# Kernel tuning notes

Hardware: AMD Instinct MI355X
Metric: run time of the kernel (lower is better)

## Reference

```python
import jax, jax.numpy as jnp
import numpy as np

B, S, DIN, DOUT, R, NL, T = 4, 4096, 1024, 1024, 16, 8, 4

def setup_inputs() -> dict:
    key = jax.random.key(0)
    k1, k2, k3, k4, k5 = jax.random.split(key, 5)
    return {
        "x": jax.random.normal(k1, (B, S, DIN), dtype=jnp.float32),
        "W": jax.random.normal(k2, (DOUT, DIN), dtype=jnp.float32) * 0.02,
        "bias": jax.random.normal(k3, (DOUT,), dtype=jnp.float32) * 0.02,
        "lora_A": jax.random.normal(k4, (NL, R, DIN), dtype=jnp.float32) * 0.02,
        "lora_B": jax.random.normal(k5, (NL, DOUT, R), dtype=jnp.float32) * 0.02,
        "tuner_index": jnp.arange(T, dtype=jnp.int64) if jax.config.jax_enable_x64 else jnp.arange(T, dtype=jnp.int32),
    }

def reference(x, W, bias, lora_A, lora_B, tuner_index):
    # Per adapter ti: F.linear(x, W + B_ti @ A_ti, bias)
    # == x @ W.T + (x @ A_ti.T) @ B_ti.T + bias  (fused low-rank form, same math)
    A = lora_A[tuner_index]   # [T, r, Din]
    Bm = lora_B[tuner_index]  # [T, Dout, r]
    base = jnp.einsum('bsd,od->bso', x, W) + bias          # [B, S, Dout]
    low = jnp.einsum('bsd,trd->tbsr', x, A)                # [T, B, S, r]
    delta = jnp.einsum('tbsr,tor->tbso', low, Bm)          # [T, B, S, Dout]
    return base[None, ...] + delta                         # [T, B, S, Dout]
```

## Files before the change

kernel.cpp:

```cpp
#include <hip/hip_runtime.h>


typedef __attribute__((ext_vector_type(8))) _Float16 f16x8;
typedef __attribute__((ext_vector_type(4))) float f32x4;
typedef __attribute__((ext_vector_type(4))) unsigned short us4;
typedef __attribute__((ext_vector_type(8))) unsigned short us8;

namespace {
constexpr int kM = 16384, kDin = 1024, kDout = 1024, kR = 16, kT = 4;
constexpr size_t OFF_XF  = 0;
constexpr size_t OFF_WF  = 33554432;
constexpr size_t OFF_LOW = 35651584;
}

__device__ inline unsigned short f2h(float f) {
  _Float16 h = (_Float16)f;
  return __builtin_bit_cast(unsigned short, h);
}
__device__ inline void gload_lds16(const void* g, void* l) {
  __builtin_amdgcn_global_load_lds(
      (const __attribute__((address_space(1))) unsigned int*)g,
      (__attribute__((address_space(3))) unsigned int*)l, 16, 0, 0);
}
__device__ inline f32x4 mfma_f16(f16x8 a, f16x8 b, f32x4 c) {
  return __builtin_amdgcn_mfma_f32_16x16x32_f16(a, b, c, 0, 0, 0);
}

__global__ __launch_bounds__(256) void lora_low(const float* __restrict__ x,
                                                const float* __restrict__ W,
                                                const float* __restrict__ A,
                                                const int* __restrict__ tuner,
                                                unsigned short* __restrict__ lowb,
                                                unsigned short* __restrict__ xf,
                                                unsigned short* __restrict__ wf) {
  {
    const int idx = blockIdx.x * 256 + threadIdx.x;
#pragma unroll
    for (int p = 0; p < 2; ++p) {
      const int j = idx + p * 131072;
      const float4 v = ((const float4*)W)[j];
      us4 h;
      h[0] = f2h(v.x); h[1] = f2h(v.y); h[2] = f2h(v.z); h[3] = f2h(v.w);
      ((us4*)wf)[j] = h;
    }
  }

  __shared__ float xs[64][34];
  __shared__ float as[64][66];
  const int tid = threadIdx.x;
  const int i0  = blockIdx.x * 32;
  const int tx  = tid & 15;
  const int ty  = tid >> 4;
  float acc[2][4] = {{0.f, 0.f, 0.f, 0.f}, {0.f, 0.f, 0.f, 0.f}};

  for (int kt = 0; kt < kDin; kt += 64) {
    __syncthreads();
#pragma unroll
    for (int p = 0; p < 2; ++p) {
      const int f = tid + p * 256;
      const int row = f >> 4, kq = (f & 15) * 4;
      const float4 v = *(const float4*)(x + (size_t)(i0 + row) * kDin + kt + kq);
      xs[kq + 0][row] = v.x; xs[kq + 1][row] = v.y;
      xs[kq + 2][row] = v.z; xs[kq + 3][row] = v.w;
      us4 h;
      h[0] = f2h(v.x); h[1] = f2h(v.y); h[2] = f2h(v.z); h[3] = f2h(v.w);
      *(us4*)(xf + (size_t)(i0 + row) * kDin + kt + kq) = h;
    }
#pragma unroll
    for (int p = 0; p < 4; ++p) {
      const int f = tid + p * 256;
      const int ar = f >> 4, kq = (f & 15) * 4;
      const int ti = tuner[ar >> 4];
      const float4 v = *(const float4*)(A + ((size_t)ti * kR + (ar & 15)) * kDin + kt + kq);
      as[kq + 0][ar] = v.x; as[kq + 1][ar] = v.y;
      as[kq + 2][ar] = v.z; as[kq + 3][ar] = v.w;
    }
    __syncthreads();
#pragma unroll 8
    for (int k = 0; k < 64; ++k) {
      const float a0 = xs[k][ty * 2], a1 = xs[k][ty * 2 + 1];
      const float b0 = as[k][tx * 4], b1 = as[k][tx * 4 + 1];
      const float b2 = as[k][tx * 4 + 2], b3 = as[k][tx * 4 + 3];
      acc[0][0] += a0 * b0; acc[0][1] += a0 * b1; acc[0][2] += a0 * b2; acc[0][3] += a0 * b3;
      acc[1][0] += a1 * b0; acc[1][1] += a1 * b1; acc[1][2] += a1 * b2; acc[1][3] += a1 * b3;
    }
  }
#pragma unroll
  for (int ii = 0; ii < 2; ++ii) {
    us4 o;
#pragma unroll
    for (int j = 0; j < 4; ++j) o[j] = f2h(acc[ii][j]);
    *(us4*)(lowb + ((size_t)(tx >> 2) * kM + i0 + ty * 2 + ii) * kR + (tx & 3) * 4) = o;
  }
}

__global__ __launch_bounds__(512) void lora_main(
    const unsigned short* __restrict__ xf, const unsigned short* __restrict__ wf,
    const float* __restrict__ bias, const float* __restrict__ Bm,
    const int* __restrict__ tuner, const unsigned short* __restrict__ lowb,
    float* __restrict__ out) {
  __shared__ __align__(16) unsigned char smem[49152];
  const int tid  = threadIdx.x;
  const int lane = tid & 63;
  const int w    = tid >> 6;

  const int swz = ((int)blockIdx.x & 7) * 64 + ((int)blockIdx.x >> 3);
  const int bm = swz >> 2, bn = swz & 3;
  const size_t i0 = (size_t)bm * 128, j0 = (size_t)bn * 256;
  const int wm = w >> 2, wn = w & 3;

  const int chsw = ((lane & 3) ^ ((lane >> 3) & 3)) * 8;
  const unsigned short* gsrc_q[3];
  int ldsoff_q[3];
#pragma unroll
  for (int q = 0; q < 3; ++q) {
    const int c = 3 * w + q;
    const bool isA = c < 8;
    const size_t rowb = (isA ? i0 + c * 16 : j0 + (c - 8) * 16) + (lane >> 2);
    gsrc_q[q] = (isA ? xf : wf) + rowb * kDin + chsw;
    ldsoff_q[q] = c * 1024;
  }

  f32x4 acc[4][4];
#pragma unroll
  for (int n = 0; n < 4; ++n)
#pragma unroll
    for (int m = 0; m < 4; ++m) acc[n][m] = (f32x4){0.f, 0.f, 0.f, 0.f};

  const int kg = lane >> 4;
  const int rl = lane & 15;
  const int csw = kg ^ ((rl >> 1) & 3);
  const int rdA = (wm * 64 + rl) * 64 + csw * 16;
  const int rdB = 8192 + (wn * 64 + rl) * 64 + csw * 16;

  auto compute_step = [&](const unsigned char* B0) {
    f16x8 a[4], b[4];
#pragma unroll
    for (int m = 0; m < 4; ++m) a[m] = *(const f16x8*)(B0 + rdA + m * 1024);
#pragma unroll
    for (int n = 0; n < 4; ++n) b[n] = *(const f16x8*)(B0 + rdB + n * 1024);
    __builtin_amdgcn_s_setprio(1);
#pragma unroll
    for (int n = 0; n < 4; ++n)
#pragma unroll
      for (int m = 0; m < 4; ++m)
        acc[n][m] = mfma_f16(b[n], a[m], acc[n][m]);
    __builtin_amdgcn_s_setprio(0);
  };

#pragma unroll
  for (int q = 0; q < 3; ++q)
    gload_lds16(gsrc_q[q], smem + ldsoff_q[q]);

  for (int s = 0; s < 31; ++s) {
    const int p = s & 1;
    {
      unsigned char* dst = smem + (p ^ 1) * 24576;
      const int ko = (s + 1) * 32;
#pragma unroll
      for (int q = 0; q < 3; ++q)
        gload_lds16(gsrc_q[q] + ko, dst + ldsoff_q[q]);
    }
    asm volatile("s_waitcnt vmcnt(3)" ::: "memory");
    __builtin_amdgcn_s_barrier();
    asm volatile("" ::: "memory");
    compute_step(smem + p * 24576);
    asm volatile("s_waitcnt lgkmcnt(0)" ::: "memory");
    __builtin_amdgcn_s_barrier();
    asm volatile("" ::: "memory");
  }
  asm volatile("s_waitcnt vmcnt(0)" ::: "memory");
  __builtin_amdgcn_s_barrier();
  asm volatile("" ::: "memory");
  compute_step(smem + 24576);

#pragma unroll
  for (int n = 0; n < 4; ++n) {
    const f32x4 bv = *(const f32x4*)(bias + j0 + wn * 64 + n * 16 + kg * 4);
#pragma unroll
    for (int m = 0; m < 4; ++m)
#pragma unroll
      for (int r = 0; r < 4; ++r) acc[n][m][r] += bv[r];
  }

  {
    const us8 z = {0, 0, 0, 0, 0, 0, 0, 0};
    if (tid < 128) {
      *(us8*)(smem + 4096 + tid * 32) = z;
      *(us8*)(smem + 4096 + tid * 32 + 16) = z;
    } else if (tid < 384) {
      *(us8*)(smem + 16384 + (tid - 128) * 32) = z;
      *(us8*)(smem + 16384 + (tid - 128) * 32 + 16) = z;
    }
  }

  for (int t = 0; t < kT; ++t) {
    __syncthreads();
    {
      const int row = tid >> 1, half = tid & 1;
      if (tid < 256) {
        const us8 lv = *(const us8*)(lowb + ((size_t)t * kM + i0 + row) * kR + half * 8);
        *(us8*)(smem + half * 2048 + row * 16) = lv;
      }
      const int ti = tuner[t];
      const float* bp = Bm + ((size_t)ti * kDout + j0 + row) * kR + half * 8;
      const float4 m0 = *(const float4*)bp;
      const float4 m1 = *(const float4*)(bp + 4);
      us8 mv;
      mv[0] = f2h(m0.x); mv[1] = f2h(m0.y); mv[2] = f2h(m0.z); mv[3] = f2h(m0.w);
      mv[4] = f2h(m1.x); mv[5] = f2h(m1.y); mv[6] = f2h(m1.z); mv[7] = f2h(m1.w);
      *(us8*)(smem + 8192 + half * 4096 + row * 16) = mv;
    }
    __syncthreads();

    f16x8 lf[4], mf[4];
#pragma unroll
    for (int m = 0; m < 4; ++m)
      lf[m] = *(const f16x8*)(smem + kg * 2048 + (wm * 64 + m * 16 + rl) * 16);
#pragma unroll
    for (int n = 0; n < 4; ++n)
      mf[n] = *(const f16x8*)(smem + 8192 + kg * 4096 + (wn * 64 + n * 16 + rl) * 16);

#pragma unroll
    for (int n = 0; n < 4; ++n)
#pragma unroll
      for (int m = 0; m < 4; ++m) {
        const f32x4 d = mfma_f16(mf[n], lf[m], acc[n][m]);
        const size_t row = (size_t)t * kM + i0 + wm * 64 + m * 16 + rl;
        const int    col = (int)j0 + wn * 64 + n * 16 + kg * 4;
        __builtin_nontemporal_store(d, (f32x4*)(out + row * kDout + col));
      }
  }
}

extern "C" void kernel_launch(void* const* d_in, const int* in_sizes, int n_in,
                              void* d_out, int out_size, void* d_ws, size_t ws_size,
                              hipStream_t stream) {
  const float* x    = (const float*)d_in[0];
  const float* W    = (const float*)d_in[1];
  const float* bias = (const float*)d_in[2];
  const float* lA   = (const float*)d_in[3];
  const float* lB   = (const float*)d_in[4];
  const int*   ti   = (const int*)d_in[5];
  float* out = (float*)d_out;

  unsigned char* ws = (unsigned char*)d_ws;
  unsigned short* xfp  = (unsigned short*)(ws + OFF_XF);
  unsigned short* wfp  = (unsigned short*)(ws + OFF_WF);
  unsigned short* lowb = (unsigned short*)(ws + OFF_LOW);

  lora_low<<<kM / 32, 256, 0, stream>>>(x, W, lA, ti, lowb, xfp, wfp);
  lora_main<<<512, 512, 0, stream>>>(xfp, wfp, bias, lB, ti, lowb, out);
}
```

Before: 161.5 us.

## Split main GEMM into 128x128 tiles with 256-thread blocks and two tiles each

The main kernel drops from 512-thread blocks computing a 128x256 output tile to 256-thread blocks that loop over two 128x128 tiles in sequence. Shared memory shrinks from 48KB to 32KB and the launch bounds ask for two blocks per CU, aiming for better occupancy and overlap between blocks. The low-rank kernel also switches to vectorized float2/float4 LDS reads with a padded A tile. In exchange, the x tile is loaded twice per block (once per column tile) and each wave keeps a 64x64 accumulator tile, so register pressure stays high.

```diff
diff --git a/kernel.cpp b/kernel.cpp
--- a/kernel.cpp
+++ b/kernel.cpp
@@ -46,7 +46,7 @@
   }
 
   __shared__ float xs[64][34];
-  __shared__ float as[64][66];
+  __shared__ float as[64][68];
   const int tid = threadIdx.x;
   const int i0  = blockIdx.x * 32;
   const int tx  = tid & 15;
@@ -76,13 +76,14 @@
       as[kq + 2][ar] = v.z; as[kq + 3][ar] = v.w;
     }
     __syncthreads();
-#pragma unroll 8
+#pragma unroll 4
     for (int k = 0; k < 64; ++k) {
-      const float a0 = xs[k][ty * 2], a1 = xs[k][ty * 2 + 1];
-      const float b0 = as[k][tx * 4], b1 = as[k][tx * 4 + 1];
-      const float b2 = as[k][tx * 4 + 2], b3 = as[k][tx * 4 + 3];
-      acc[0][0] += a0 * b0; acc[0][1] += a0 * b1; acc[0][2] += a0 * b2; acc[0][3] += a0 * b3;
-      acc[1][0] += a1 * b0; acc[1][1] += a1 * b1; acc[1][2] += a1 * b2; acc[1][3] += a1 * b3;
+      const float2 xv = *(const float2*)&xs[k][ty * 2];
+      const float4 av = *(const float4*)&as[k][tx * 4];
+      acc[0][0] += xv.x * av.x; acc[0][1] += xv.x * av.y;
+      acc[0][2] += xv.x * av.z; acc[0][3] += xv.x * av.w;
+      acc[1][0] += xv.y * av.x; acc[1][1] += xv.y * av.y;
+      acc[1][2] += xv.y * av.z; acc[1][3] += xv.y * av.w;
     }
   }
 #pragma unroll
@@ -94,142 +95,143 @@
   }
 }
 
-__global__ __launch_bounds__(512) void lora_main(
+__global__ __launch_bounds__(256, 2) void lora_main(
     const unsigned short* __restrict__ xf, const unsigned short* __restrict__ wf,
     const float* __restrict__ bias, const float* __restrict__ Bm,
     const int* __restrict__ tuner, const unsigned short* __restrict__ lowb,
     float* __restrict__ out) {
-  __shared__ __align__(16) unsigned char smem[49152];
+  __shared__ __align__(16) unsigned char smem[32768];
   const int tid  = threadIdx.x;
   const int lane = tid & 63;
   const int w    = tid >> 6;
 
   const int swz = ((int)blockIdx.x & 7) * 64 + ((int)blockIdx.x >> 3);
-  const int bm = swz >> 2, bn = swz & 3;
-  const size_t i0 = (size_t)bm * 128, j0 = (size_t)bn * 256;
-  const int wm = w >> 2, wn = w & 3;
+  const int bm = swz >> 2, bn2 = swz & 3;
+  const size_t i0 = (size_t)bm * 128;
+  const int wm = w >> 1, wn = w & 1;
 
   const int chsw = ((lane & 3) ^ ((lane >> 3) & 3)) * 8;
-  const unsigned short* gsrc_q[3];
-  int ldsoff_q[3];
-#pragma unroll
-  for (int q = 0; q < 3; ++q) {
-    const int c = 3 * w + q;
-    const bool isA = c < 8;
-    const size_t rowb = (isA ? i0 + c * 16 : j0 + (c - 8) * 16) + (lane >> 2);
-    gsrc_q[q] = (isA ? xf : wf) + rowb * kDin + chsw;
-    ldsoff_q[q] = c * 1024;
-  }
-
-  f32x4 acc[4][4];
-#pragma unroll
-  for (int n = 0; n < 4; ++n)
-#pragma unroll
-    for (int m = 0; m < 4; ++m) acc[n][m] = (f32x4){0.f, 0.f, 0.f, 0.f};
-
   const int kg = lane >> 4;
   const int rl = lane & 15;
   const int csw = kg ^ ((rl >> 1) & 3);
   const int rdA = (wm * 64 + rl) * 64 + csw * 16;
   const int rdB = 8192 + (wn * 64 + rl) * 64 + csw * 16;
 
-  auto compute_step = [&](const unsigned char* B0) {
-    f16x8 a[4], b[4];
-#pragma unroll
-    for (int m = 0; m < 4; ++m) a[m] = *(const f16x8*)(B0 + rdA + m * 1024);
-#pragma unroll
-    for (int n = 0; n < 4; ++n) b[n] = *(const f16x8*)(B0 + rdB + n * 1024);
-    __builtin_amdgcn_s_setprio(1);
+#pragma unroll 1
+  for (int tt = 0; tt < 2; ++tt) {
+    const size_t j0 = (size_t)(bn2 + 4 * tt) * 128;
+
+    const unsigned short* gsrc_q[4];
+    int ldsoff_q[4];
+#pragma unroll
+    for (int q = 0; q < 4; ++q) {
+      const int c = 4 * w + q;
+      const bool isA = c < 8;
+      const size_t rowb = (isA ? i0 + c * 16 : j0 + (c - 8) * 16) + (lane >> 2);
+      gsrc_q[q] = (isA ? xf : wf) + rowb * kDin + chsw;
+      ldsoff_q[q] = c * 1024;
+    }
+
+    f32x4 acc[4][4];
 #pragma unroll
     for (int n = 0; n < 4; ++n)
 #pragma unroll
-      for (int m = 0; m < 4; ++m)
-        acc[n][m] = mfma_f16(b[n], a[m], acc[n][m]);
-    __builtin_amdgcn_s_setprio(0);
-  };
-
-#pragma unroll
-  for (int q = 0; q < 3; ++q)
-    gload_lds16(gsrc_q[q], smem + ldsoff_q[q]);
-
-  for (int s = 0; s < 31; ++s) {
-    const int p = s & 1;
-    {
-      unsigned char* dst = smem + (p ^ 1) * 24576;
-      const int ko = (s + 1) * 32;
-#pragma unroll
-      for (int q = 0; q < 3; ++q)
-        gload_lds16(gsrc_q[q] + ko, dst + ldsoff_q[q]);
-    }
-    asm volatile("s_waitcnt vmcnt(3)" ::: "memory");
+      for (int m = 0; m < 4; ++m) acc[n][m] = (f32x4){0.f, 0.f, 0.f, 0.f};
+
+    auto compute_step = [&](const unsigned char* B0) {
+      f16x8 a[4], b[4];
+#pragma unroll
+      for (int m = 0; m < 4; ++m) a[m] = *(const f16x8*)(B0 + rdA + m * 1024);
+#pragma unroll
+      for (int n = 0; n < 4; ++n) b[n] = *(const f16x8*)(B0 + rdB + n * 1024);
+      __builtin_amdgcn_s_setprio(1);
+#pragma unroll
+      for (int n = 0; n < 4; ++n)
+#pragma unroll
+        for (int m = 0; m < 4; ++m)
+          acc[n][m] = mfma_f16(b[n], a[m], acc[n][m]);
+      __builtin_amdgcn_s_setprio(0);
+    };
+
+#pragma unroll
+    for (int q = 0; q < 4; ++q)
+      gload_lds16(gsrc_q[q], smem + ldsoff_q[q]);
+
+    for (int s = 0; s < 31; ++s) {
+      const int p = s & 1;
+      {
+        unsigned char* dst = smem + (p ^ 1) * 16384;
+        const int ko = (s + 1) * 32;
+#pragma unroll
+        for (int q = 0; q < 4; ++q)
+          gload_lds16(gsrc_q[q] + ko, dst + ldsoff_q[q]);
+      }
+      asm volatile("s_waitcnt vmcnt(4)" ::: "memory");
+      __builtin_amdgcn_s_barrier();
+      asm volatile("" ::: "memory");
+      compute_step(smem + p * 16384);
+      asm volatile("s_waitcnt lgkmcnt(0)" ::: "memory");
+      __builtin_amdgcn_s_barrier();
+      asm volatile("" ::: "memory");
+    }
+    asm volatile("s_waitcnt vmcnt(0)" ::: "memory");
     __builtin_amdgcn_s_barrier();
     asm volatile("" ::: "memory");
-    compute_step(smem + p * 24576);
-    asm volatile("s_waitcnt lgkmcnt(0)" ::: "memory");
-    __builtin_amdgcn_s_barrier();
-    asm volatile("" ::: "memory");
-  }
-  asm volatile("s_waitcnt vmcnt(0)" ::: "memory");
-  __builtin_amdgcn_s_barrier();
-  asm volatile("" ::: "memory");
-  compute_step(smem + 24576);
-
-#pragma unroll
-  for (int n = 0; n < 4; ++n) {
-    const f32x4 bv = *(const f32x4*)(bias + j0 + wn * 64 + n * 16 + kg * 4);
-#pragma unroll
-    for (int m = 0; m < 4; ++m)
-#pragma unroll
-      for (int r = 0; r < 4; ++r) acc[n][m][r] += bv[r];
-  }
-
-  {
-    const us8 z = {0, 0, 0, 0, 0, 0, 0, 0};
-    if (tid < 128) {
-      *(us8*)(smem + 4096 + tid * 32) = z;
-      *(us8*)(smem + 4096 + tid * 32 + 16) = z;
-    } else if (tid < 384) {
-      *(us8*)(smem + 16384 + (tid - 128) * 32) = z;
-      *(us8*)(smem + 16384 + (tid - 128) * 32 + 16) = z;
-    }
-  }
-
-  for (int t = 0; t < kT; ++t) {
-    __syncthreads();
+    compute_step(smem + 16384);
+
+#pragma unroll
+    for (int n = 0; n < 4; ++n) {
+      const f32x4 bv = *(const f32x4*)(bias + j0 + wn * 64 + n * 16 + kg * 4);
+#pragma unroll
+      for (int m = 0; m < 4; ++m)
+#pragma unroll
+        for (int r = 0; r < 4; ++r) acc[n][m][r] += bv[r];
+    }
+
     {
-      const int row = tid >> 1, half = tid & 1;
-      if (tid < 256) {
+      const us8 z = {0, 0, 0, 0, 0, 0, 0, 0};
+      unsigned char* p = (tid < 128) ? (smem + 4096 + tid * 32)
+                                     : (smem + 12288 + (tid - 128) * 32);
+      *(us8*)p = z;
+      *(us8*)(p + 16) = z;
+    }
+
+    for (int t = 0; t < kT; ++t) {
+      __syncthreads();
+      {
+        const int row = tid >> 1, half = tid & 1;
         const us8 lv = *(const us8*)(lowb + ((size_t)t * kM + i0 + row) * kR + half * 8);
         *(us8*)(smem + half * 2048 + row * 16) = lv;
+        const int ti = tuner[t];
+        const float* bp = Bm + ((size_t)ti * kDout + j0 + row) * kR + half * 8;
+        const float4 m0 = *(const float4*)bp;
+        const float4 m1 = *(const float4*)(bp + 4);
+        us8 mv;
+        mv[0] = f2h(m0.x); mv[1] = f2h(m0.y); mv[2] = f2h(m0.z); mv[3] = f2h(m0.w);
+        mv[4] = f2h(m1.x); mv[5] = f2h(m1.y); mv[6] = f2h(m1.z); mv[7] = f2h(m1.w);
+        *(us8*)(smem + 8192 + half * 2048 + row * 16) = mv;
       }
-      const int ti = tuner[t];
-      const float* bp = Bm + ((size_t)ti * kDout + j0 + row) * kR + half * 8;
-      const float4 m0 = *(const float4*)bp;
-      const float4 m1 = *(const float4*)(bp + 4);
-      us8 mv;
-      mv[0] = f2h(m0.x); mv[1] = f2h(m0.y); mv[2] = f2h(m0.z); mv[3] = f2h(m0.w);
-      mv[4] = f2h(m1.x); mv[5] = f2h(m1.y); mv[6] = f2h(m1.z); mv[7] = f2h(m1.w);
-      *(us8*)(smem + 8192 + half * 4096 + row * 16) = mv;
+      __syncthreads();
+
+      f16x8 lf[4], mf[4];
+#pragma unroll
+      for (int m = 0; m < 4; ++m)
+        lf[m] = *(const f16x8*)(smem + kg * 2048 + (wm * 64 + m * 16 + rl) * 16);
+#pragma unroll
+      for (int n = 0; n < 4; ++n)
+        mf[n] = *(const f16x8*)(smem + 8192 + kg * 2048 + (wn * 64 + n * 16 + rl) * 16);
+
+#pragma unroll
+      for (int n = 0; n < 4; ++n)
+#pragma unroll
+        for (int m = 0; m < 4; ++m) {
+          const f32x4 d = mfma_f16(mf[n], lf[m], acc[n][m]);
+          const size_t row = (size_t)t * kM + i0 + wm * 64 + m * 16 + rl;
+          const int    col = (int)j0 + wn * 64 + n * 16 + kg * 4;
+          __builtin_nontemporal_store(d, (f32x4*)(out + row * kDout + col));
+        }
     }
     __syncthreads();
-
-    f16x8 lf[4], mf[4];
-#pragma unroll
-    for (int m = 0; m < 4; ++m)
-      lf[m] = *(const f16x8*)(smem + kg * 2048 + (wm * 64 + m * 16 + rl) * 16);
-#pragma unroll
-    for (int n = 0; n < 4; ++n)
-      mf[n] = *(const f16x8*)(smem + 8192 + kg * 4096 + (wn * 64 + n * 16 + rl) * 16);
-
-#pragma unroll
-    for (int n = 0; n < 4; ++n)
-#pragma unroll
-      for (int m = 0; m < 4; ++m) {
-        const f32x4 d = mfma_f16(mf[n], lf[m], acc[n][m]);
-        const size_t row = (size_t)t * kM + i0 + wm * 64 + m * 16 + rl;
-        const int    col = (int)j0 + wn * 64 + n * 16 + kg * 4;
-        __builtin_nontemporal_store(d, (f32x4*)(out + row * kDout + col));
-      }
   }
 }
 
@@ -250,5 +252,5 @@
   unsigned short* lowb = (unsigned short*)(ws + OFF_LOW);
 
   lora_low<<<kM / 32, 256, 0, stream>>>(x, W, lA, ti, lowb, xfp, wfp);
-  lora_main<<<512, 512, 0, stream>>>(xfp, wfp, bias, lB, ti, lowb, out);
-}
+  lora_main<<<512, 256, 0, stream>>>(xfp, wfp, bias, lB, ti, lowb, out);
+}
```

Result: slower. 172.5 us (+6.8%).
